# Optimization experiments

Hardware: AMD Instinct MI355X
Metric: run time of the kernel (lower is better)

## Reference

```python
import jax, jax.numpy as jnp
import numpy as np
import math

DIM = 1024
ATTN_DIM = 1024
B, S = 2, 4096

def setup_inputs() -> dict:
    key = jax.random.key(0)
    k1, k2, k3 = jax.random.split(key, 3)
    x = jax.random.normal(k1, (B, S, DIM), dtype=jnp.float32)
    # qkv Linear(dim, 3*attn_dim, bias=True): weight [3*attn_dim, dim], bias [3*attn_dim]
    W_qkv = jax.random.normal(k2, (3 * ATTN_DIM, DIM), dtype=jnp.float32) * (1.0 / math.sqrt(DIM))
    b_qkv = jax.random.normal(k3, (3 * ATTN_DIM,), dtype=jnp.float32) * 0.01
    return {"x": x, "W_qkv": W_qkv, "b_qkv": b_qkv}

def reference(x, W_qkv, b_qkv):
    b, s, d = x.shape
    qkv = jnp.einsum('bsd,ed->bse', x, W_qkv) + b_qkv  # [B,S,3*attn_dim]
    q, k, v = jnp.split(qkv, 3, axis=-1)
    score = jnp.einsum('bqd,bkd->bqk', q, k)  # [B,S,S]
    # causal mask applied BEFORE scaling (matches original: -inf survives the divide)
    causal = jnp.tril(jnp.ones((s, s), dtype=bool))
    score = jnp.where(causal, score, -jnp.inf)
    attn = jax.nn.softmax(score / math.sqrt(ATTN_DIM), axis=-1)
    y = jnp.einsum('bqk,bkd->bqd', attn, v)  # [B,S,attn_dim]
    return y
```

## Files before the change

kernel.cpp:

```cpp
#include <hip/hip_runtime.h>
#include <cstdint>
#include <cstddef>

typedef __bf16 bf16;
typedef bf16 bf16x4 __attribute__((ext_vector_type(4)));
typedef bf16 bf16x8 __attribute__((ext_vector_type(8)));
typedef float f32x4 __attribute__((ext_vector_type(4)));

#define SEQ 4096
#define DIMD 1024
#define TILE_K1024 131072L
#define TILE_K4096 524288L
#define PC_BATCH   8650752L

__device__ __forceinline__ int swz(int r, int c) {
    return r * 32 + (((((c >> 3) ^ (r >> 1)) & 3)) << 3) + (c & 7);
}

__device__ __forceinline__ void async16(void* lds, const void* g) {
    __builtin_amdgcn_global_load_lds(
        (__attribute__((address_space(1))) void*)g,
        (__attribute__((address_space(3))) void*)lds,
        16, 0, 0);
}

__device__ __forceinline__ void gemm_core(
    const bf16* __restrict__ At, const bf16* __restrict__ Bt,
    int k0, int k1, f32x4 acc[4][4])
{
    __shared__ bf16 lt[2][2][4096];
    const int tid  = threadIdx.x;
    const int lane = tid & 63;
    const int wid  = tid >> 6;
    const int wm   = (wid >> 1) * 64;
    const int wn   = (wid & 1) * 64;
    const int lr   = lane & 15;
    const int q    = lane >> 4;

    int offA[4], offB[4];
#pragma unroll
    for (int mi = 0; mi < 4; ++mi) {
        const int rA = wm + mi * 16 + lr;
        offA[mi] = rA * 32 + ((((rA >> 1) ^ q) & 3) << 3);
    }
#pragma unroll
    for (int ni = 0; ni < 4; ++ni) {
        const int rB = wn + ni * 16 + lr;
        offB[ni] = rB * 32 + ((((rB >> 1) ^ q) & 3) << 3);
    }

    const int t8 = tid * 8;

#define STAGE(kk, c) do { \
        const bf16* _sa = At + (long)(kk) * 4096; \
        const bf16* _sb = Bt + (long)(kk) * 4096; \
        async16(&lt[c][0][t8],        _sa + t8); \
        async16(&lt[c][0][2048 + t8], _sa + 2048 + t8); \
        async16(&lt[c][1][t8],        _sb + t8); \
        async16(&lt[c][1][2048 + t8], _sb + 2048 + t8); \
    } while (0)

    STAGE(k0, 0);
    if (k0 + 1 < k1) STAGE(k0 + 1, 1);

    for (int kk = k0; kk < k1; ++kk) {
        const int cur = (kk - k0) & 1;
        if (kk + 1 < k1) { asm volatile("s_waitcnt vmcnt(4)" ::: "memory"); }
        else             { asm volatile("s_waitcnt vmcnt(0)" ::: "memory"); }
        __builtin_amdgcn_s_barrier();
        __builtin_amdgcn_sched_barrier(0);

        bf16x8 af[4], bfr[4];
#pragma unroll
        for (int mi = 0; mi < 4; ++mi)
            af[mi] = *(const bf16x8*)&lt[cur][0][offA[mi]];
#pragma unroll
        for (int ni = 0; ni < 4; ++ni)
            bfr[ni] = *(const bf16x8*)&lt[cur][1][offB[ni]];

        __builtin_amdgcn_s_setprio(1);
#pragma unroll
        for (int mi = 0; mi < 4; ++mi)
#pragma unroll
            for (int ni = 0; ni < 4; ++ni)
                acc[mi][ni] = __builtin_amdgcn_mfma_f32_16x16x32_bf16(
                    af[mi], bfr[ni], acc[mi][ni], 0, 0, 0);
        __builtin_amdgcn_s_setprio(0);
        __builtin_amdgcn_sched_barrier(0);
        __builtin_amdgcn_s_barrier();
        if (kk + 2 < k1) STAGE(kk + 2, cur);
    }
#undef STAGE
}

__global__ __launch_bounds__(256) void cvt_all_kernel(
    const float* __restrict__ x, const float* __restrict__ W,
    bf16* __restrict__ xt, bf16* __restrict__ wt, float* __restrict__ sums)
{
    const int g = blockIdx.x, tid = threadIdx.x;
    if (g >= 11264) { sums[(g - 11264) * 256 + tid] = 0.0f; return; }
    const float* in; bf16* out; int i;
    if (g < 8192) { in = x; out = xt; i = g * 256 + tid; }
    else          { in = W; out = wt; i = (g - 8192) * 256 + tid; }
    const float4 v = ((const float4*)in)[i];
    const int j = i * 4, row = j >> 10, col = j & 1023;
    const long o = (long)(row >> 7) * TILE_K1024 + (col >> 5) * 4096
                 + swz(row & 127, col & 31);
    bf16x4 ov = { (bf16)v.x, (bf16)v.y, (bf16)v.z, (bf16)v.w };
    *(bf16x4*)&out[o] = ov;
}

__global__ __launch_bounds__(256) void qkv_gemm(
    const bf16* __restrict__ xt, const bf16* __restrict__ wt,
    const float* __restrict__ bias,
    bf16* __restrict__ Qt, bf16* __restrict__ Kt, bf16* __restrict__ Vtt)
{
    const int b = blockIdx.x, x = b & 7, r = b >> 3;
    const int mt = x * 8 + r / 24, wnid = r % 24;
    const int bm = mt * 128, bn = wnid * 128;

    f32x4 acc[4][4] = {};
    gemm_core(xt + (long)mt * TILE_K1024, wt + (long)wnid * TILE_K1024, 0, 32, acc);

    const int tid = threadIdx.x, lane = tid & 63, wid = tid >> 6;
    const int wm = (wid >> 1) * 64, wn = (wid & 1) * 64;
    const int lr = lane & 15, q4 = (lane >> 4) * 4;
#pragma unroll
    for (int ni = 0; ni < 4; ++ni) {
        const int n = bn + wn + ni * 16 + lr;
        const float bv = bias[n];
#pragma unroll
        for (int mi = 0; mi < 4; ++mi) {
            const int m0 = bm + wm + mi * 16 + q4;
            if (n < 2048) {
                bf16* dst = (n < 1024) ? Qt : Kt;
                const int c = n & 1023;
#pragma unroll
                for (int rr = 0; rr < 4; ++rr) {
                    const int m = m0 + rr;
                    dst[(long)(m >> 7) * TILE_K1024 + (c >> 5) * 4096
                        + swz(m & 127, c & 31)] = (bf16)(acc[mi][ni][rr] + bv);
                }
            } else {
                const int bb = m0 >> 12, s = m0 & 4095, d = n - 2048;
                bf16x4 o = { (bf16)(acc[mi][ni][0] + bv), (bf16)(acc[mi][ni][1] + bv),
                             (bf16)(acc[mi][ni][2] + bv), (bf16)(acc[mi][ni][3] + bv) };
                *(bf16x4*)&Vtt[(long)bb * 4194304 + (long)(d >> 7) * TILE_K4096
                               + (s >> 5) * 4096 + swz(d & 127, s & 31)] = o;
            }
        }
    }
}

__global__ __launch_bounds__(256) void score_kernel(
    const bf16* __restrict__ Qt, const bf16* __restrict__ Kt,
    bf16* __restrict__ Pc, float* __restrict__ sums)
{
    const int b = blockIdx.x, x = b & 7;
    int r = b >> 3;
    const int bz = r / 66, batch = bz;
    r %= 66;
    int qt, kt;
    const int s0 = x + 1;
    if (r < s0)           { qt = x;      kt = r; }
    else if (r < 33)      { qt = 31 - x; kt = r - s0; }
    else if (r < 42 + x)  { qt = x + 8;  kt = r - 33; }
    else                  { qt = 23 - x; kt = r - 42 - x; }

    bf16* Pb = Pc + (long)bz * PC_BATCH + (long)(qt * (qt + 1) / 2 + kt) * 16384;
    float* sb = sums + (long)batch * SEQ;

    f32x4 acc[4][4] = {};
    gemm_core(Kt + (long)(batch * 32 + kt) * TILE_K1024,
              Qt + (long)(batch * 32 + qt) * TILE_K1024,
              0, 32, acc);

    const int tid = threadIdx.x, lane = tid & 63, wid = tid >> 6;
    const int wm = (wid >> 1) * 64, wn = (wid & 1) * 64;
    const int lr = lane & 15, q4 = (lane >> 4) * 4;
#pragma unroll
    for (int ni = 0; ni < 4; ++ni) {
        const int ql = wn + ni * 16 + lr;
        const int q  = qt * 128 + ql;
        float rsum = 0.0f;
#pragma unroll
        for (int mi = 0; mi < 4; ++mi) {
            const int kl0  = wm + mi * 16 + q4;
            const int key0 = kt * 128 + kl0;
            bf16x4 o;
#pragma unroll
            for (int rr = 0; rr < 4; ++rr) {
                const float s = acc[mi][ni][rr] * 0.03125f;
                const float p = (key0 + rr <= q) ? __expf(s) : 0.0f;
                o[rr] = (bf16)p;
                rsum += (float)o[rr];
            }
            *(bf16x4*)&Pb[(kl0 >> 5) * 4096 + swz(ql, kl0 & 31)] = o;
        }
        rsum += __shfl_xor(rsum, 16);
        rsum += __shfl_xor(rsum, 32);
        if (lane < 16) atomicAdd(&sb[q], rsum);
    }
}

__device__ const unsigned char pv_sched[96] = {
     15, 125,  28,  44,  25,  54,  86,  51,  83, 112,   4,   3,
     47,  93,  60,  12,  57,  22, 118,  19, 115,  80,  36,  35,
     31,  61,  92, 122,  89, 119,  10,  41,  18,  48,   5,   2,
     63,  29, 124,  90, 121,  87,  42,   9,  50,  16,  37,  34,
     95,  46,  13,  58,  24,  55,  21, 116,  82, 113,   7,   0,
    127,  14,  45,  26,  56,  23,  53,  84, 114,  81,  39,  32,
     30, 126,  27, 123,  88,  43,  85,  52,   8,  49,   6,   1,
     62,  94,  59,  91, 120,  11, 117,  20,  40,  17,  38,  33,
};

__global__ __launch_bounds__(256) void pv_kernel(
    const bf16* __restrict__ Pc, const bf16* __restrict__ Vtt,
    const float* __restrict__ sums, float* __restrict__ Y,
    float* __restrict__ part)
{
    const int b = blockIdx.x, x = b & 7, t = b >> 3;
    const int j = t >> 3, dt = t & 7;
    const int e = pv_sched[x * 12 + j];
    const int qt = e & 31, bz = (e >> 5) & 1, c = e >> 6;
    const int full = (qt + 1) * 4, half = (qt + 1) * 2;
    int k0, k1;
    if (qt < 16) { k0 = 0; k1 = full; }
    else { k0 = c ? half : 0; k1 = c ? full : half; }
    const int batch = bz;

    f32x4 acc[4][4] = {};
    gemm_core(Pc + (long)bz * PC_BATCH + (long)(qt * (qt + 1) / 2) * 16384,
              Vtt + (long)batch * 4194304 + (long)dt * TILE_K4096, k0, k1, acc);

    const int tid = threadIdx.x, lane = tid & 63, wid = tid >> 6;
    const int wm = (wid >> 1) * 64, wn = (wid & 1) * 64;
    const int lr = lane & 15, q4 = (lane >> 4) * 4;
#pragma unroll
    for (int mi = 0; mi < 4; ++mi) {
#pragma unroll
        for (int rr = 0; rr < 4; ++rr) {
            const int q = qt * 128 + wm + mi * 16 + q4 + rr;
            const float iv = 1.0f / sums[(long)batch * SEQ + q];
#pragma unroll
            for (int ni = 0; ni < 4; ++ni) {
                const int d = dt * 128 + wn + ni * 16 + lr;
                const float v = acc[mi][ni][rr] * iv;
                if (c == 0)
                    Y[(long)batch * 4194304 + (long)q * DIMD + d] = v;
                else
                    part[(long)bz * 2097152 + (long)(q - 2048) * DIMD + d] = v;
            }
        }
    }
}

__global__ __launch_bounds__(256) void combine_kernel(
    float* __restrict__ Y, const float* __restrict__ part)
{
    const long g = (long)blockIdx.x * 256 + threadIdx.x;
    const long e4 = g * 4;
    const int bz = (int)(e4 >> 21);
    const long rem = e4 & 2097151;
    float4 a = *(const float4*)&Y[(long)bz * 4194304 + 2097152 + rem];
    const float4 p = *(const float4*)&part[e4];
    a.x += p.x; a.y += p.y; a.z += p.z; a.w += p.w;
    *(float4*)&Y[(long)bz * 4194304 + 2097152 + rem] = a;
}

extern "C" void kernel_launch(void* const* d_in, const int* in_sizes, int n_in,
                              void* d_out, int out_size, void* d_ws, size_t ws_size,
                              hipStream_t stream)
{
    const float* x    = (const float*)d_in[0];
    const float* W    = (const float*)d_in[1];
    const float* bqkv = (const float*)d_in[2];
    float* out = (float*)d_out;
    char* ws = (char*)d_ws;

    bf16* Pc   = (bf16*)ws;
    bf16* xt   = (bf16*)ws;
    bf16* wt   = (bf16*)(ws + 16 * 1024 * 1024);
    bf16* Kt   = (bf16*)(ws + 34603008);
    bf16* Vtt  = (bf16*)(ws + 51380224);
    float* sums = (float*)(ws + 68157440);
    bf16* Qt   = (bf16*)d_out;
    float* part = (float*)Kt;

    cvt_all_kernel<<<11296, 256, 0, stream>>>(x, W, xt, wt, sums);
    qkv_gemm<<<1536, 256, 0, stream>>>(xt, wt, bqkv, Qt, Kt, Vtt);
    score_kernel<<<1056, 256, 0, stream>>>(Qt, Kt, Pc, sums);
    pv_kernel<<<768, 256, 0, stream>>>(Pc, Vtt, sums, out, part);
    combine_kernel<<<4096, 256, 0, stream>>>(out, part);
}
```

Baseline: 235.8 us.

## Fuse split-K combine into pv kernel via per-tile arrival flags

Removes the separate combine kernel by having the two split-K halves of each long query tile coordinate through an atomic ticket. The first arriving block writes its normalized partial to a scratch buffer and publishes a flag, and the second block spins on that flag, then adds the partial to its own result and writes Y directly. This saves one kernel launch and a full read-modify-write pass over half of Y. In exchange it adds a spin-wait that could stall or deadlock if the partner block is not resident, plus fence and flag overhead.

```diff
diff --git a/kernel.cpp b/kernel.cpp
--- a/kernel.cpp
+++ b/kernel.cpp
@@ -95,10 +95,15 @@
 
 __global__ __launch_bounds__(256) void cvt_all_kernel(
     const float* __restrict__ x, const float* __restrict__ W,
-    bf16* __restrict__ xt, bf16* __restrict__ wt, float* __restrict__ sums)
+    bf16* __restrict__ xt, bf16* __restrict__ wt, float* __restrict__ sums,
+    int* __restrict__ flags)
 {
     const int g = blockIdx.x, tid = threadIdx.x;
-    if (g >= 11264) { sums[(g - 11264) * 256 + tid] = 0.0f; return; }
+    if (g >= 11264) {
+        if (g == 11296) { flags[tid] = 0; flags[tid + 256] = 0; }
+        else            { sums[(g - 11264) * 256 + tid] = 0.0f; }
+        return;
+    }
     const float* in; bf16* out; int i;
     if (g < 8192) { in = x; out = xt; i = g * 256 + tid; }
     else          { in = W; out = wt; i = (g - 8192) * 256 + tid; }
@@ -217,7 +222,7 @@
 __global__ __launch_bounds__(256) void pv_kernel(
     const bf16* __restrict__ Pc, const bf16* __restrict__ Vtt,
     const float* __restrict__ sums, float* __restrict__ Y,
-    float* __restrict__ part)
+    float* __restrict__ part, int* __restrict__ flags)
 {
     const int b = blockIdx.x, x = b & 7, t = b >> 3;
     const int j = t >> 3, dt = t & 7;
@@ -236,36 +241,68 @@
     const int tid = threadIdx.x, lane = tid & 63, wid = tid >> 6;
     const int wm = (wid >> 1) * 64, wn = (wid & 1) * 64;
     const int lr = lane & 15, q4 = (lane >> 4) * 4;
-#pragma unroll
-    for (int mi = 0; mi < 4; ++mi) {
-#pragma unroll
-        for (int rr = 0; rr < 4; ++rr) {
-            const int q = qt * 128 + wm + mi * 16 + q4 + rr;
-            const float iv = 1.0f / sums[(long)batch * SEQ + q];
-#pragma unroll
-            for (int ni = 0; ni < 4; ++ni) {
-                const int d = dt * 128 + wn + ni * 16 + lr;
-                const float v = acc[mi][ni][rr] * iv;
-                if (c == 0)
-                    Y[(long)batch * 4194304 + (long)q * DIMD + d] = v;
-                else
-                    part[(long)bz * 2097152 + (long)(q - 2048) * DIMD + d] = v;
-            }
-        }
-    }
-}
-
-__global__ __launch_bounds__(256) void combine_kernel(
-    float* __restrict__ Y, const float* __restrict__ part)
-{
-    const long g = (long)blockIdx.x * 256 + threadIdx.x;
-    const long e4 = g * 4;
-    const int bz = (int)(e4 >> 21);
-    const long rem = e4 & 2097151;
-    float4 a = *(const float4*)&Y[(long)bz * 4194304 + 2097152 + rem];
-    const float4 p = *(const float4*)&part[e4];
-    a.x += p.x; a.y += p.y; a.z += p.z; a.w += p.w;
-    *(float4*)&Y[(long)bz * 4194304 + 2097152 + rem] = a;
+
+    if (qt < 16) {
+#pragma unroll
+        for (int mi = 0; mi < 4; ++mi) {
+#pragma unroll
+            for (int rr = 0; rr < 4; ++rr) {
+                const int q = qt * 128 + wm + mi * 16 + q4 + rr;
+                const float iv = 1.0f / sums[(long)batch * SEQ + q];
+#pragma unroll
+                for (int ni = 0; ni < 4; ++ni) {
+                    const int d = dt * 128 + wn + ni * 16 + lr;
+                    Y[(long)batch * 4194304 + (long)q * DIMD + d] = acc[mi][ni][rr] * iv;
+                }
+            }
+        }
+        return;
+    }
+
+    const int g = ((bz << 4) | (qt - 16)) * 8 + dt;
+    __shared__ int tk;
+    if (tid == 0) tk = atomicAdd(&flags[g], 1);
+    __syncthreads();
+
+    if (tk == 0) {
+#pragma unroll
+        for (int mi = 0; mi < 4; ++mi) {
+#pragma unroll
+            for (int rr = 0; rr < 4; ++rr) {
+                const int q = qt * 128 + wm + mi * 16 + q4 + rr;
+                const float iv = 1.0f / sums[(long)batch * SEQ + q];
+#pragma unroll
+                for (int ni = 0; ni < 4; ++ni) {
+                    const int d = dt * 128 + wn + ni * 16 + lr;
+                    part[(long)bz * 2097152 + (long)(q - 2048) * DIMD + d]
+                        = acc[mi][ni][rr] * iv;
+                }
+            }
+        }
+        __threadfence();
+        __syncthreads();
+        if (tid == 0) atomicExch(&flags[256 + g], 1);
+    } else {
+        if (tid == 0) { while (atomicAdd(&flags[256 + g], 0) == 0) {} }
+        __syncthreads();
+        __threadfence();
+#pragma unroll
+        for (int mi = 0; mi < 4; ++mi) {
+#pragma unroll
+            for (int rr = 0; rr < 4; ++rr) {
+                const int q = qt * 128 + wm + mi * 16 + q4 + rr;
+                const float iv = 1.0f / sums[(long)batch * SEQ + q];
+#pragma unroll
+                for (int ni = 0; ni < 4; ++ni) {
+                    const int d = dt * 128 + wn + ni * 16 + lr;
+                    const float other =
+                        part[(long)bz * 2097152 + (long)(q - 2048) * DIMD + d];
+                    Y[(long)batch * 4194304 + (long)q * DIMD + d]
+                        = other + acc[mi][ni][rr] * iv;
+                }
+            }
+        }
+    }
 }
 
 extern "C" void kernel_launch(void* const* d_in, const int* in_sizes, int n_in,
@@ -284,12 +321,12 @@
     bf16* Kt   = (bf16*)(ws + 34603008);
     bf16* Vtt  = (bf16*)(ws + 51380224);
     float* sums = (float*)(ws + 68157440);
+    int* flags  = (int*)(ws + 68190208);
     bf16* Qt   = (bf16*)d_out;
     float* part = (float*)Kt;
 
-    cvt_all_kernel<<<11296, 256, 0, stream>>>(x, W, xt, wt, sums);
+    cvt_all_kernel<<<11297, 256, 0, stream>>>(x, W, xt, wt, sums, flags);
     qkv_gemm<<<1536, 256, 0, stream>>>(xt, wt, bqkv, Qt, Kt, Vtt);
     score_kernel<<<1056, 256, 0, stream>>>(Qt, Kt, Pc, sums);
-    pv_kernel<<<768, 256, 0, stream>>>(Pc, Vtt, sums, out, part);
-    combine_kernel<<<4096, 256, 0, stream>>>(out, part);
-}
+    pv_kernel<<<768, 256, 0, stream>>>(Pc, Vtt, sums, out, part, flags);
+}
```

Result: slower. 324.9 us (+37.8%).
